# Performance work log

Hardware: AMD Instinct MI355X
Metric: run time of the kernel (lower is better)

The kernel has to match this reference:

```python
import jax, jax.numpy as jnp
import numpy as np

HIDDEN = 1024
ATTN = 1024
B, S = 4, 2048


def setup_inputs() -> dict:
    key = jax.random.key(0)
    ks = jax.random.split(key, 6)
    bound = 1.0 / np.sqrt(HIDDEN)
    return {
        "query": jax.random.normal(ks[0], (B, S, HIDDEN), jnp.float32),
        "value": jax.random.normal(ks[1], (B, S, HIDDEN), jnp.float32),
        "Wq": jax.random.uniform(ks[2], (HIDDEN, ATTN), jnp.float32, -bound, bound),
        "bq": jax.random.uniform(ks[3], (ATTN,), jnp.float32, -bound, bound),
        "Wv": jax.random.uniform(ks[4], (HIDDEN, ATTN), jnp.float32, -bound, bound),
        "bv": jax.random.uniform(ks[5], (ATTN,), jnp.float32, -bound, bound),
    }


def reference(query, value, Wq, bq, Wv, bv):
    # Linear projections (torch Linear: x @ W^T + b; here W stored as [in, out])
    q = jnp.einsum("bsh,hd->bsd", query, Wq) + bq  # [B,S,ATTN]
    v = jnp.einsum("bsh,hd->bsd", value, Wv) + bv  # [B,S,ATTN]
    # Unscaled dot-product attention
    scores = jnp.einsum("bqd,bkd->bqk", q, v)       # [B,S,S]
    attn = jax.nn.softmax(scores, axis=-1)
    context = jnp.einsum("bqk,bkd->bqd", attn, v)   # [B,S,ATTN]
    return context
```

## Files before the change

### kernel.cpp

```cpp
#include <hip/hip_runtime.h>
#include <hip/hip_bf16.h>


typedef unsigned short u16;
typedef __attribute__((ext_vector_type(8))) short bf16x8;
typedef __attribute__((ext_vector_type(4))) float f32x4;

typedef __attribute__((address_space(1))) void gvoid_t;
typedef __attribute__((address_space(3))) void svoid_t;

__device__ __forceinline__ void gll16(const void* g, void* l) {
    __builtin_amdgcn_global_load_lds((gvoid_t*)g, (svoid_t*)l, 16, 0, 0);
}

__device__ __forceinline__ u16 bf16rn(float x) {
    unsigned u = __float_as_uint(x);
    unsigned r = (u + 0x7FFFu + ((u >> 16) & 1u)) >> 16;
    return (u16)r;
}
__device__ __forceinline__ float bf2f(u16 h) {
    return __uint_as_float(((unsigned)h) << 16);
}

__device__ __forceinline__ const char* sel3(const char* p0, const char* p1,
                                            const char* p2, int i) {
    return i == 0 ? p0 : (i == 1 ? p1 : p2);
}

#define NSK 48

#define STAGE_A(T, mh) {                                                      \
    const char* _p = sel3(A0z, A1z, A2z, (T) >> 4) + (long)((T) & 15) * 128;  \
    char* _d = smem + (((T) & 1) << 16) + ((mh) << 14) + (w << 10);           \
    gll16(_p + offA##mh##0, _d);                                              \
    gll16(_p + offA##mh##1, _d + 8192); }

#define STAGE_B(T, nh) {                                                      \
    const char* _p = sel3(B0z, B1z, B2z, (T) >> 4) + (long)((T) & 15) * 128;  \
    char* _d = smem + (((T) & 1) << 16) + 32768 + ((nh) << 14) + (w << 10);   \
    gll16(_p + offB##nh##0, _d);                                              \
    gll16(_p + offB##nh##1, _d + 8192); }

#define VM4 { asm volatile("s_waitcnt vmcnt(4)" ::: "memory");                \
              __builtin_amdgcn_sched_barrier(0); }
#define VM0 { asm volatile("s_waitcnt vmcnt(0)" ::: "memory");                \
              __builtin_amdgcn_sched_barrier(0); }

#define PHASE(mh, nh, RDA, RDB, BFR, STAGE, ENDW)                             \
  {                                                                           \
    if (RDA) {                                                                \
      _Pragma("unroll") for (int mi = 0; mi < 4; ++mi)                        \
        _Pragma("unroll") for (int ks = 0; ks < 2; ++ks)                      \
          afr[mi][ks] = *(const bf16x8*)(smem + bufb + ((mh) << 14) +         \
              aRdB + mi * 2048 + csw[ks]);                                    \
    }                                                                         \
    if (RDB) {                                                                \
      _Pragma("unroll") for (int ni = 0; ni < 2; ++ni)                        \
        _Pragma("unroll") for (int ks = 0; ks < 2; ++ks)                      \
          BFR[ni][ks] = *(const bf16x8*)(smem + bufb + ((nh) << 14) +         \
              bRdB + ni * 2048 + csw[ks]);                                    \
    }                                                                         \
    STAGE;                                                                    \
    __builtin_amdgcn_s_barrier();                                             \
    asm volatile("s_waitcnt lgkmcnt(0)" ::: "memory");                        \
    __builtin_amdgcn_sched_barrier(0);                                        \
    __builtin_amdgcn_s_setprio(1);                                            \
    _Pragma("unroll") for (int mi = 0; mi < 4; ++mi)                          \
      _Pragma("unroll") for (int ni = 0; ni < 2; ++ni)                        \
        _Pragma("unroll") for (int ks = 0; ks < 2; ++ks)                      \
          acc[(mh) * 4 + mi][(nh) * 2 + ni] =                                 \
              __builtin_amdgcn_mfma_f32_16x16x32_bf16(                        \
                  afr[mi][ks], BFR[ni][ks],                                   \
                  acc[(mh) * 4 + mi][(nh) * 2 + ni], 0, 0, 0);                \
    __builtin_amdgcn_s_setprio(0);                                            \
    ENDW;                                                                     \
    __builtin_amdgcn_s_barrier();                                             \
  }

template<bool OUTF32, int SCHEME>
__global__ __launch_bounds__(512, 2)
void gemm8(const char* a0, const char* a1, const char* a2, long zA,
           const char* b0, const char* b1, const char* b2, long zB,
           float* __restrict__ Of, u16* __restrict__ Ohi, u16* __restrict__ Olo,
           long zC, const float* __restrict__ bias0,
           const float* __restrict__ bias1, int N)
{
    extern __shared__ char smem[];
    const int t = threadIdx.x, lane = t & 63, w = t >> 6;
    const int wm = w >> 2, wn = w & 3;

    const int bid = blockIdx.x;
    const int xcd = bid & 7, bi = bid >> 3;
    int m0, n0, z;
    if (SCHEME == 0) {
        z = xcd >> 1;
        m0 = (((xcd & 1) << 2) | (bi >> 3)) << 8;
        n0 = (bi & 7) << 8;
    } else {
        m0 = ((xcd << 2) | (bi >> 3)) << 8;
        n0 = (bi & 3) << 8;
        z = (bi >> 2) & 1;
    }

    const char* A0z = a0 + (long)z * zA;
    const char* A1z = a1 + (long)z * zA;
    const char* A2z = a2 + (long)z * zA;
    const char* B0z = b0 + (long)z * zB;
    const char* B1z = b1 + (long)z * zB;
    const char* B2z = b2 + (long)z * zB;

    const int lr0 = t >> 3;
    const long cg = (long)((((t & 7) ^ ((t >> 3) & 7)) << 4));
    const long offA00 = (long)(m0 + lr0) * 2048 + cg;
    const long offA01 = offA00 + 128L * 2048;
    const long offA10 = (long)(m0 + 64 + lr0) * 2048 + cg;
    const long offA11 = offA10 + 128L * 2048;
    const long offB00 = (long)(n0 + ((lr0 >> 5) << 6) + (lr0 & 31)) * 2048 + cg;
    const long offB01 = offB00 + 128L * 2048;
    const long offB10 = offB00 + 32L * 2048;
    const long offB11 = offB10 + 128L * 2048;

    const int swl = (lane & 7) << 4;
    const int csw[2] = { (((lane >> 4) << 4)) ^ swl,
                         (((lane >> 4) << 4) + 64) ^ swl };
    const int aRdB = (wm * 64 + (lane & 15)) * 128;
    const int bRdB = 32768 + (wn * 32 + (lane & 15)) * 128;

    f32x4 acc[8][4];
#pragma unroll
    for (int i = 0; i < 8; ++i)
#pragma unroll
        for (int j = 0; j < 4; ++j) acc[i][j] = (f32x4)0.f;
    bf16x8 afr[4][2];
    bf16x8 b0r[2][2], b1r[2][2];

    STAGE_A(0, 0); STAGE_B(0, 0); STAGE_A(0, 1); STAGE_B(0, 1);
    STAGE_A(1, 0); STAGE_B(1, 0);
    asm volatile("s_waitcnt vmcnt(4)" ::: "memory");
    __builtin_amdgcn_sched_barrier(0);
    __builtin_amdgcn_s_barrier();

    for (int s = 0; s < NSK - 2; ++s) {
        const int bufb = (s & 1) << 16;
        PHASE(0, 0, 1, 1, b0r, STAGE_A(s + 1, 1), );
        PHASE(0, 1, 0, 1, b1r, STAGE_B(s + 1, 1), );
        PHASE(1, 0, 1, 0, b0r, STAGE_A(s + 2, 0), );
        PHASE(1, 1, 0, 0, b1r, STAGE_B(s + 2, 0), VM4);
    }
    {
        const int bufb = ((NSK - 2) & 1) << 16;
        PHASE(0, 0, 1, 1, b0r, STAGE_A(NSK - 1, 1), );
        PHASE(0, 1, 0, 1, b1r, STAGE_B(NSK - 1, 1), );
        PHASE(1, 0, 1, 0, b0r, , );
        PHASE(1, 1, 0, 0, b1r, , VM0);
    }
    {
        const int bufb = ((NSK - 1) & 1) << 16;
        PHASE(0, 0, 1, 1, b0r, , );
        PHASE(0, 1, 0, 1, b1r, , );
        PHASE(1, 0, 1, 0, b0r, , );
        PHASE(1, 1, 0, 0, b1r, , );
    }

    const int r0 = m0 + wm * 128 + ((lane >> 4) << 2);
    const int c0 = n0 + wn * 64 + (lane & 15);
    if (OUTF32) {
        float* Co = Of + (long)z * zC;
#pragma unroll
        for (int mi = 0; mi < 8; ++mi)
#pragma unroll
            for (int nj = 0; nj < 4; ++nj)
#pragma unroll
                for (int r = 0; r < 4; ++r)
                    Co[(long)(r0 + mi * 16 + r) * N + c0 + nj * 16] =
                        acc[mi][nj][r];
    } else {
        const float* bs = z ? bias1 : bias0;
        float bc[4];
#pragma unroll
        for (int nj = 0; nj < 4; ++nj) bc[nj] = bs[c0 + nj * 16];
        u16* Oh = Ohi + (long)z * zC;
        u16* Ol = Olo + (long)z * zC;
#pragma unroll
        for (int mi = 0; mi < 8; ++mi)
#pragma unroll
            for (int nj = 0; nj < 4; ++nj)
#pragma unroll
                for (int r = 0; r < 4; ++r) {
                    float x = acc[mi][nj][r] + bc[nj];
                    long o = (long)(r0 + mi * 16 + r) * N + c0 + nj * 16;
                    u16 h = bf16rn(x);
                    Oh[o] = h;
                    Ol[o] = bf16rn(x - bf2f(h));
                }
    }
}

#define PVNSK 64

#define PV_STAGE_A(T, mh) {                                                   \
    const char* _p = Ap + (long)((T) & 31) * 128;                             \
    char* _d = smem + (((T) & 1) * 49152) + ((mh) << 14) + (w << 10);         \
    gll16(_p + offA##mh##0, _d);                                              \
    gll16(_p + offA##mh##1, _d + 8192); }

#define PV_STAGE_B(T, nh) {                                                   \
    const char* _p = (((T) >> 5) ? Bl : Bh) + (long)((T) & 31) * 128;         \
    char* _d = smem + (((T) & 1) * 49152) + 32768 + ((nh) << 13) + (w << 10); \
    gll16(_p + offB##nh, _d); }

#define PVM3 { asm volatile("s_waitcnt vmcnt(3)" ::: "memory");               \
               __builtin_amdgcn_sched_barrier(0); }

#define PVPHASE(mh, nh, RDA, RDB, BFR, STAGE, ENDW)                           \
  {                                                                           \
    if (RDA) {                                                                \
      _Pragma("unroll") for (int mi = 0; mi < 4; ++mi)                        \
        _Pragma("unroll") for (int ks = 0; ks < 2; ++ks)                      \
          afr[mi][ks] = *(const bf16x8*)(smem + bufb + ((mh) << 14) +         \
              aRdB + mi * 2048 + csw[ks]);                                    \
    }                                                                         \
    if (RDB) {                                                                \
      _Pragma("unroll") for (int ks = 0; ks < 2; ++ks)                        \
        BFR[ks] = *(const bf16x8*)(smem + bufb + 32768 + ((nh) << 13) +       \
            bRdB + csw[ks]);                                                  \
    }                                                                         \
    STAGE;                                                                    \
    __builtin_amdgcn_s_barrier();                                             \
    asm volatile("s_waitcnt lgkmcnt(0)" ::: "memory");                        \
    __builtin_amdgcn_sched_barrier(0);                                        \
    __builtin_amdgcn_s_setprio(1);                                            \
    _Pragma("unroll") for (int mi = 0; mi < 4; ++mi)                          \
      _Pragma("unroll") for (int ks = 0; ks < 2; ++ks)                        \
        acc[(mh) * 4 + mi][nh] =                                              \
            __builtin_amdgcn_mfma_f32_16x16x32_bf16(                          \
                afr[mi][ks], BFR[ks], acc[(mh) * 4 + mi][nh], 0, 0, 0);       \
    __builtin_amdgcn_s_setprio(0);                                            \
    ENDW;                                                                     \
    __builtin_amdgcn_s_barrier();                                             \
  }

__global__ __launch_bounds__(512, 2)
void gemm8pv(const char* pA, const char* vTh, const char* vTl,
             float* __restrict__ Of)
{
    extern __shared__ char smem[];
    const int t = threadIdx.x, lane = t & 63, w = t >> 6;
    const int wm = w >> 2, wn = w & 3;

    const int bid = blockIdx.x;
    const int xcd = bid & 7, bi = bid >> 3;
    const int z  = xcd >> 1;
    const int m0 = ((((xcd & 1) << 2) | (bi >> 3)) << 8);
    const int n0 = (bi & 7) << 7;

    const char* Ap = pA  + (long)z * 8388608;
    const char* Bh = vTh + (long)z * 4194304;
    const char* Bl = vTl + (long)z * 4194304;

    const int lr0 = t >> 3;
    const long cg = (long)((((t & 7) ^ ((t >> 3) & 7)) << 4));
    const long offA00 = (long)(m0 + lr0) * 4096 + cg;
    const long offA01 = offA00 + 64L * 4096;
    const long offA10 = (long)(m0 + 128 + lr0) * 4096 + cg;
    const long offA11 = offA10 + 64L * 4096;
    const long offB0  = (long)(n0 + lr0) * 4096 + cg;
    const long offB1  = (long)(n0 + 64 + lr0) * 4096 + cg;

    const int swl = (lane & 7) << 4;
    const int csw[2] = { (((lane >> 4) << 4)) ^ swl,
                         (((lane >> 4) << 4) + 64) ^ swl };
    const int aRdB = (wm * 64 + (lane & 15)) * 128;
    const int bRdB = (wn * 16 + (lane & 15)) * 128;

    f32x4 acc[8][2];
#pragma unroll
    for (int i = 0; i < 8; ++i) { acc[i][0] = (f32x4)0.f; acc[i][1] = (f32x4)0.f; }
    bf16x8 afr[4][2];
    bf16x8 bA[2], bB[2];

    PV_STAGE_A(0, 0); PV_STAGE_B(0, 0); PV_STAGE_A(0, 1); PV_STAGE_B(0, 1);
    PV_STAGE_A(1, 0); PV_STAGE_B(1, 0);
    asm volatile("s_waitcnt vmcnt(3)" ::: "memory");
    __builtin_amdgcn_sched_barrier(0);
    __builtin_amdgcn_s_barrier();

    for (int s = 0; s < PVNSK - 2; ++s) {
        const int bufb = (s & 1) * 49152;
        PVPHASE(0, 0, 1, 1, bA, PV_STAGE_A(s + 1, 1), );
        PVPHASE(0, 1, 0, 1, bB, PV_STAGE_B(s + 1, 1), );
        PVPHASE(1, 0, 1, 0, bA, PV_STAGE_A(s + 2, 0), );
        PVPHASE(1, 1, 0, 0, bB, PV_STAGE_B(s + 2, 0), PVM3);
    }
    {
        const int bufb = ((PVNSK - 2) & 1) * 49152;
        PVPHASE(0, 0, 1, 1, bA, PV_STAGE_A(PVNSK - 1, 1), );
        PVPHASE(0, 1, 0, 1, bB, PV_STAGE_B(PVNSK - 1, 1), );
        PVPHASE(1, 0, 1, 0, bA, , );
        PVPHASE(1, 1, 0, 0, bB, , VM0);
    }
    {
        const int bufb = ((PVNSK - 1) & 1) * 49152;
        PVPHASE(0, 0, 1, 1, bA, , );
        PVPHASE(0, 1, 0, 1, bB, , );
        PVPHASE(1, 0, 1, 0, bA, , );
        PVPHASE(1, 1, 0, 0, bB, , );
    }

    float* Co = Of + (long)z * 2097152;
    const int r0 = m0 + wm * 64 + ((lane >> 4) << 2);
    const int c0 = n0 + wn * 16 + (lane & 15);
#pragma unroll
    for (int mh = 0; mh < 2; ++mh)
#pragma unroll
        for (int mi = 0; mi < 4; ++mi)
#pragma unroll
            for (int nh = 0; nh < 2; ++nh)
#pragma unroll
                for (int r = 0; r < 4; ++r)
                    Co[(long)(r0 + mh * 128 + mi * 16 + r) * 1024 +
                       c0 + nh * 64] = acc[mh * 4 + mi][nh][r];
}

__global__ __launch_bounds__(256)
void split2_f32(const float* __restrict__ q, const float* __restrict__ v,
                u16* __restrict__ qh, u16* __restrict__ ql,
                u16* __restrict__ vh, u16* __restrict__ vl)
{
    const int sel = blockIdx.y;
    const float* in = sel ? v : q;
    u16* hi = sel ? vh : qh;
    u16* lo = sel ? vl : ql;
    long i = ((long)blockIdx.x * 256 + threadIdx.x) * 4;
    float4 x = *(const float4*)(in + i);
    ushort4 h, l;
    h.x = bf16rn(x.x); l.x = bf16rn(x.x - bf2f(h.x));
    h.y = bf16rn(x.y); l.y = bf16rn(x.y - bf2f(h.y));
    h.z = bf16rn(x.z); l.z = bf16rn(x.z - bf2f(h.z));
    h.w = bf16rn(x.w); l.w = bf16rn(x.w - bf2f(h.w));
    *(ushort4*)(hi + i) = h;
    *(ushort4*)(lo + i) = l;
}

__global__ __launch_bounds__(256)
void tsplit2_w(const float* __restrict__ Wq, const float* __restrict__ Wv,
               u16* __restrict__ qhi, u16* __restrict__ qlo,
               u16* __restrict__ vhi, u16* __restrict__ vlo)
{
    __shared__ float tile[32][33];
    const int sel = blockIdx.z;
    const float* W = sel ? Wv : Wq;
    u16* hi = sel ? vhi : qhi;
    u16* lo = sel ? vlo : qlo;
    const int n0v = blockIdx.x * 32, k0 = blockIdx.y * 32;
    const int r = threadIdx.x >> 5, c = threadIdx.x & 31;
#pragma unroll
    for (int it = 0; it < 4; ++it)
        tile[r + it * 8][c] = W[(long)(k0 + r + it * 8) * 1024 + n0v + c];
    __syncthreads();
#pragma unroll
    for (int it = 0; it < 4; ++it) {
        const int rr = r + it * 8;
        float x = tile[c][rr];
        u16 h = bf16rn(x);
        long o = (long)(n0v + rr) * 1024 + k0 + c;
        hi[o] = h;
        lo[o] = bf16rn(x - bf2f(h));
    }
}

__global__ __launch_bounds__(256)
void tr2_bf16(const u16* __restrict__ v_hi, const u16* __restrict__ v_lo,
              u16* __restrict__ vT_hi, u16* __restrict__ vT_lo)
{
    __shared__ u16 tile[64][68];
    const int pl = blockIdx.z & 1, b = blockIdx.z >> 1;
    const u16* src = (pl ? v_lo : v_hi) + (long)b * 2097152;
    u16* dst = (pl ? vT_lo : vT_hi) + (long)b * 2097152;
    const int s0 = blockIdx.x * 64, d0 = blockIdx.y * 64;
    const int t = threadIdx.x;
    const int rr = t >> 4, c4 = (t & 15) * 4;
#pragma unroll
    for (int it = 0; it < 4; ++it) {
        const int s = it * 16 + rr;
        *(short4*)&tile[s][c4] =
            *(const short4*)(src + (long)(s0 + s) * 1024 + d0 + c4);
    }
    __syncthreads();
#pragma unroll
    for (int it = 0; it < 4; ++it) {
        const int d = it * 16 + rr;
        short4 o;
        o.x = tile[c4 + 0][d]; o.y = tile[c4 + 1][d];
        o.z = tile[c4 + 2][d]; o.w = tile[c4 + 3][d];
        *(short4*)(dst + (long)(d0 + d) * 2048 + s0 + c4) = o;
    }
}

__global__ __launch_bounds__(256)
void softmax_p(const float* __restrict__ S, u16* __restrict__ P)
{
    const float* p = S + (long)blockIdx.x * 2048;
    u16* o = P + (long)blockIdx.x * 2048;
    const int t = threadIdx.x;

    float4 x0 = *(const float4*)&p[t * 4];
    float4 x1 = *(const float4*)&p[1024 + t * 4];

    float mx = fmaxf(fmaxf(fmaxf(x0.x, x0.y), fmaxf(x0.z, x0.w)),
                     fmaxf(fmaxf(x1.x, x1.y), fmaxf(x1.z, x1.w)));
#pragma unroll
    for (int off = 32; off; off >>= 1) mx = fmaxf(mx, __shfl_xor(mx, off));

    __shared__ float red[8];
    if ((t & 63) == 0) red[t >> 6] = mx;
    __syncthreads();
    mx = fmaxf(fmaxf(red[0], red[1]), fmaxf(red[2], red[3]));

    x0.x = __expf(x0.x - mx); x0.y = __expf(x0.y - mx);
    x0.z = __expf(x0.z - mx); x0.w = __expf(x0.w - mx);
    x1.x = __expf(x1.x - mx); x1.y = __expf(x1.y - mx);
    x1.z = __expf(x1.z - mx); x1.w = __expf(x1.w - mx);

    float sm2 = (x0.x + x0.y + x0.z + x0.w) + (x1.x + x1.y + x1.z + x1.w);
#pragma unroll
    for (int off = 32; off; off >>= 1) sm2 += __shfl_xor(sm2, off);
    if ((t & 63) == 0) red[4 + (t >> 6)] = sm2;
    __syncthreads();
    sm2 = (red[4] + red[5]) + (red[6] + red[7]);

    const float inv = 1.0f / sm2;
    ushort4 y;
    y.x = bf16rn(x0.x * inv); y.y = bf16rn(x0.y * inv);
    y.z = bf16rn(x0.z * inv); y.w = bf16rn(x0.w * inv);
    *(ushort4*)(o + t * 4) = y;
    y.x = bf16rn(x1.x * inv); y.y = bf16rn(x1.y * inv);
    y.z = bf16rn(x1.z * inv); y.w = bf16rn(x1.w * inv);
    *(ushort4*)(o + 1024 + t * 4) = y;
}

extern "C" void kernel_launch(void* const* d_in, const int* in_sizes, int n_in,
                              void* d_out, int out_size, void* d_ws, size_t ws_size,
                              hipStream_t stream)
{
    const float* query = (const float*)d_in[0];
    const float* value = (const float*)d_in[1];
    const float* Wq    = (const float*)d_in[2];
    const float* bq    = (const float*)d_in[3];
    const float* Wv    = (const float*)d_in[4];
    const float* bv    = (const float*)d_in[5];
    float* out = (float*)d_out;

    char* W = (char*)d_ws;
    u16* qx_hi = (u16*)(W);
    u16* qx_lo = qx_hi + 8388608;
    u16* vx_hi = qx_lo + 8388608;
    u16* vx_lo = vx_hi + 8388608;
    float* sc  = (float*)W;
    u16* q_hi  = (u16*)(W + 67108864);
    u16* q_lo  = q_hi + 8388608;
    u16* p     = (u16*)(W + 67108864);
    u16* v_hi  = (u16*)(W + 100663296);
    u16* v_lo  = v_hi + 8388608;
    u16* vT_hi = (u16*)(W + 134217728);
    u16* vT_lo = vT_hi + 8388608;
    u16* WqT_hi = (u16*)(W + 167772160);
    u16* WqT_lo = WqT_hi + 1048576;
    u16* WvT_hi = WqT_lo + 1048576;
    u16* WvT_lo = WvT_hi + 1048576;

    hipFuncSetAttribute((const void*)&gemm8<false, 1>,
                        hipFuncAttributeMaxDynamicSharedMemorySize, 131072);
    hipFuncSetAttribute((const void*)&gemm8<true, 0>,
                        hipFuncAttributeMaxDynamicSharedMemorySize, 131072);
    hipFuncSetAttribute((const void*)&gemm8pv,
                        hipFuncAttributeMaxDynamicSharedMemorySize, 98304);

    split2_f32<<<dim3(8192, 2), 256, 0, stream>>>(query, value,
                                                  qx_hi, qx_lo, vx_hi, vx_lo);
    tsplit2_w<<<dim3(32, 32, 2), 256, 0, stream>>>(Wq, Wv,
                                                   WqT_hi, WqT_lo, WvT_hi, WvT_lo);

    gemm8<false, 1><<<256, 512, 131072, stream>>>(
        (const char*)qx_hi, (const char*)qx_hi, (const char*)qx_lo, 33554432L,
        (const char*)WqT_hi, (const char*)WqT_lo, (const char*)WqT_hi, 4194304L,
        nullptr, q_hi, q_lo, 16777216L, bq, bv, 1024);

    tr2_bf16<<<dim3(32, 16, 8), 256, 0, stream>>>(v_hi, v_lo, vT_hi, vT_lo);

    gemm8<true, 0><<<256, 512, 131072, stream>>>(
        (const char*)q_hi, (const char*)q_hi, (const char*)q_lo, 4194304L,
        (const char*)v_hi, (const char*)v_lo, (const char*)v_hi, 4194304L,
        sc, nullptr, nullptr, 4194304L, nullptr, nullptr, 2048);

    softmax_p<<<8192, 256, 0, stream>>>(sc, p);

    gemm8pv<<<256, 512, 98304, stream>>>(
        (const char*)p, (const char*)vT_hi, (const char*)vT_lo, out);
}
```

Measured before the change: 393.5 us.

## Cut per-phase barriers in GEMM main loops to two per k-step

Replaces the four-phase structure, which had two workgroup barriers and an explicit LDS wait per phase, with straight-line reads, staging and MFMA quads. Each k-step now has only two barriers: one midway, before the second-half prefetch overwrites the half-buffer already consumed, and one at the end after the vmcnt wait. The LDS read waits are left to the compiler. This lowers barrier stalls and lets LDS reads overlap MFMAs, but it depends on the remaining barriers being enough to prevent write-after-read races on the shared buffers.

```diff
diff --git a/kernel.cpp b/kernel.cpp
--- a/kernel.cpp
+++ b/kernel.cpp
@@ -46,24 +46,19 @@
 #define VM0 { asm volatile("s_waitcnt vmcnt(0)" ::: "memory");                \
               __builtin_amdgcn_sched_barrier(0); }
 
-#define PHASE(mh, nh, RDA, RDB, BFR, STAGE, ENDW)                             \
-  {                                                                           \
-    if (RDA) {                                                                \
-      _Pragma("unroll") for (int mi = 0; mi < 4; ++mi)                        \
-        _Pragma("unroll") for (int ks = 0; ks < 2; ++ks)                      \
-          afr[mi][ks] = *(const bf16x8*)(smem + bufb + ((mh) << 14) +         \
-              aRdB + mi * 2048 + csw[ks]);                                    \
-    }                                                                         \
-    if (RDB) {                                                                \
-      _Pragma("unroll") for (int ni = 0; ni < 2; ++ni)                        \
-        _Pragma("unroll") for (int ks = 0; ks < 2; ++ks)                      \
-          BFR[ni][ks] = *(const bf16x8*)(smem + bufb + ((nh) << 14) +         \
-              bRdB + ni * 2048 + csw[ks]);                                    \
-    }                                                                         \
-    STAGE;                                                                    \
-    __builtin_amdgcn_s_barrier();                                             \
-    asm volatile("s_waitcnt lgkmcnt(0)" ::: "memory");                        \
-    __builtin_amdgcn_sched_barrier(0);                                        \
+#define RD_A(mh)                                                              \
+    _Pragma("unroll") for (int mi = 0; mi < 4; ++mi)                          \
+      _Pragma("unroll") for (int ks = 0; ks < 2; ++ks)                        \
+        afr[mi][ks] = *(const bf16x8*)(smem + bufb + ((mh) << 14) +           \
+            aRdB + mi * 2048 + csw[ks]);
+
+#define RD_B(BFR, nh)                                                         \
+    _Pragma("unroll") for (int ni = 0; ni < 2; ++ni)                          \
+      _Pragma("unroll") for (int ks = 0; ks < 2; ++ks)                        \
+        BFR[ni][ks] = *(const bf16x8*)(smem + bufb + ((nh) << 14) +           \
+            bRdB + ni * 2048 + csw[ks]);
+
+#define MFMA_Q(mh, nh, BFR) {                                                 \
     __builtin_amdgcn_s_setprio(1);                                            \
     _Pragma("unroll") for (int mi = 0; mi < 4; ++mi)                          \
       _Pragma("unroll") for (int ni = 0; ni < 2; ++ni)                        \
@@ -72,10 +67,7 @@
               __builtin_amdgcn_mfma_f32_16x16x32_bf16(                        \
                   afr[mi][ks], BFR[ni][ks],                                   \
                   acc[(mh) * 4 + mi][(nh) * 2 + ni], 0, 0, 0);                \
-    __builtin_amdgcn_s_setprio(0);                                            \
-    ENDW;                                                                     \
-    __builtin_amdgcn_s_barrier();                                             \
-  }
+    __builtin_amdgcn_s_setprio(0); }
 
 template<bool OUTF32, int SCHEME>
 __global__ __launch_bounds__(512, 2)
@@ -142,24 +134,44 @@
 
     for (int s = 0; s < NSK - 2; ++s) {
         const int bufb = (s & 1) << 16;
-        PHASE(0, 0, 1, 1, b0r, STAGE_A(s + 1, 1), );
-        PHASE(0, 1, 0, 1, b1r, STAGE_B(s + 1, 1), );
-        PHASE(1, 0, 1, 0, b0r, STAGE_A(s + 2, 0), );
-        PHASE(1, 1, 0, 0, b1r, STAGE_B(s + 2, 0), VM4);
+        RD_A(0); RD_B(b0r, 0);
+        STAGE_A(s + 1, 1);
+        MFMA_Q(0, 0, b0r);
+        RD_B(b1r, 1);
+        STAGE_B(s + 1, 1);
+        MFMA_Q(0, 1, b1r);
+        __builtin_amdgcn_s_barrier();
+        RD_A(1);
+        STAGE_A(s + 2, 0);
+        MFMA_Q(1, 0, b0r);
+        STAGE_B(s + 2, 0);
+        MFMA_Q(1, 1, b1r);
+        VM4;
+        __builtin_amdgcn_s_barrier();
     }
     {
         const int bufb = ((NSK - 2) & 1) << 16;
-        PHASE(0, 0, 1, 1, b0r, STAGE_A(NSK - 1, 1), );
-        PHASE(0, 1, 0, 1, b1r, STAGE_B(NSK - 1, 1), );
-        PHASE(1, 0, 1, 0, b0r, , );
-        PHASE(1, 1, 0, 0, b1r, , VM0);
+        RD_A(0); RD_B(b0r, 0);
+        STAGE_A(NSK - 1, 1);
+        MFMA_Q(0, 0, b0r);
+        RD_B(b1r, 1);
+        STAGE_B(NSK - 1, 1);
+        MFMA_Q(0, 1, b1r);
+        RD_A(1);
+        MFMA_Q(1, 0, b0r);
+        MFMA_Q(1, 1, b1r);
+        VM0;
+        __builtin_amdgcn_s_barrier();
     }
     {
         const int bufb = ((NSK - 1) & 1) << 16;
-        PHASE(0, 0, 1, 1, b0r, , );
-        PHASE(0, 1, 0, 1, b1r, , );
-        PHASE(1, 0, 1, 0, b0r, , );
-        PHASE(1, 1, 0, 0, b1r, , );
+        RD_A(0); RD_B(b0r, 0);
+        MFMA_Q(0, 0, b0r);
+        RD_B(b1r, 1);
+        MFMA_Q(0, 1, b1r);
+        RD_A(1);
+        MFMA_Q(1, 0, b0r);
+        MFMA_Q(1, 1, b1r);
     }
 
     const int r0 = m0 + wm * 128 + ((lane >> 4) << 2);
@@ -212,33 +224,25 @@
 #define PVM3 { asm volatile("s_waitcnt vmcnt(3)" ::: "memory");               \
                __builtin_amdgcn_sched_barrier(0); }
 
-#define PVPHASE(mh, nh, RDA, RDB, BFR, STAGE, ENDW)                           \
-  {                                                                           \
-    if (RDA) {                                                                \
-      _Pragma("unroll") for (int mi = 0; mi < 4; ++mi)                        \
-        _Pragma("unroll") for (int ks = 0; ks < 2; ++ks)                      \
-          afr[mi][ks] = *(const bf16x8*)(smem + bufb + ((mh) << 14) +         \
-              aRdB + mi * 2048 + csw[ks]);                                    \
-    }                                                                         \
-    if (RDB) {                                                                \
+#define PV_RD_A(mh)                                                           \
+    _Pragma("unroll") for (int mi = 0; mi < 4; ++mi)                          \
       _Pragma("unroll") for (int ks = 0; ks < 2; ++ks)                        \
-        BFR[ks] = *(const bf16x8*)(smem + bufb + 32768 + ((nh) << 13) +       \
-            bRdB + csw[ks]);                                                  \
-    }                                                                         \
-    STAGE;                                                                    \
-    __builtin_amdgcn_s_barrier();                                             \
-    asm volatile("s_waitcnt lgkmcnt(0)" ::: "memory");                        \
-    __builtin_amdgcn_sched_barrier(0);                                        \
+        afr[mi][ks] = *(const bf16x8*)(smem + bufb + ((mh) << 14) +           \
+            aRdB + mi * 2048 + csw[ks]);
+
+#define PV_RD_B(BFR, nh)                                                      \
+    _Pragma("unroll") for (int ks = 0; ks < 2; ++ks)                          \
+      BFR[ks] = *(const bf16x8*)(smem + bufb + 32768 + ((nh) << 13) +         \
+          bRdB + csw[ks]);
+
+#define PV_MFMA_Q(mh, nh, BFR) {                                              \
     __builtin_amdgcn_s_setprio(1);                                            \
     _Pragma("unroll") for (int mi = 0; mi < 4; ++mi)                          \
       _Pragma("unroll") for (int ks = 0; ks < 2; ++ks)                        \
         acc[(mh) * 4 + mi][nh] =                                              \
             __builtin_amdgcn_mfma_f32_16x16x32_bf16(                          \
                 afr[mi][ks], BFR[ks], acc[(mh) * 4 + mi][nh], 0, 0, 0);       \
-    __builtin_amdgcn_s_setprio(0);                                            \
-    ENDW;                                                                     \
-    __builtin_amdgcn_s_barrier();                                             \
-  }
+    __builtin_amdgcn_s_setprio(0); }
 
 __global__ __launch_bounds__(512, 2)
 void gemm8pv(const char* pA, const char* vTh, const char* vTl,
@@ -287,24 +291,44 @@
 
     for (int s = 0; s < PVNSK - 2; ++s) {
         const int bufb = (s & 1) * 49152;
-        PVPHASE(0, 0, 1, 1, bA, PV_STAGE_A(s + 1, 1), );
-        PVPHASE(0, 1, 0, 1, bB, PV_STAGE_B(s + 1, 1), );
-        PVPHASE(1, 0, 1, 0, bA, PV_STAGE_A(s + 2, 0), );
-        PVPHASE(1, 1, 0, 0, bB, PV_STAGE_B(s + 2, 0), PVM3);
+        PV_RD_A(0); PV_RD_B(bA, 0);
+        PV_STAGE_A(s + 1, 1);
+        PV_MFMA_Q(0, 0, bA);
+        PV_RD_B(bB, 1);
+        PV_STAGE_B(s + 1, 1);
+        PV_MFMA_Q(0, 1, bB);
+        __builtin_amdgcn_s_barrier();
+        PV_RD_A(1);
+        PV_STAGE_A(s + 2, 0);
+        PV_MFMA_Q(1, 0, bA);
+        PV_STAGE_B(s + 2, 0);
+        PV_MFMA_Q(1, 1, bB);
+        PVM3;
+        __builtin_amdgcn_s_barrier();
     }
     {
         const int bufb = ((PVNSK - 2) & 1) * 49152;
-        PVPHASE(0, 0, 1, 1, bA, PV_STAGE_A(PVNSK - 1, 1), );
-        PVPHASE(0, 1, 0, 1, bB, PV_STAGE_B(PVNSK - 1, 1), );
-        PVPHASE(1, 0, 1, 0, bA, , );
-        PVPHASE(1, 1, 0, 0, bB, , VM0);
+        PV_RD_A(0); PV_RD_B(bA, 0);
+        PV_STAGE_A(PVNSK - 1, 1);
+        PV_MFMA_Q(0, 0, bA);
+        PV_RD_B(bB, 1);
+        PV_STAGE_B(PVNSK - 1, 1);
+        PV_MFMA_Q(0, 1, bB);
+        PV_RD_A(1);
+        PV_MFMA_Q(1, 0, bA);
+        PV_MFMA_Q(1, 1, bB);
+        VM0;
+        __builtin_amdgcn_s_barrier();
     }
     {
         const int bufb = ((PVNSK - 1) & 1) * 49152;
-        PVPHASE(0, 0, 1, 1, bA, , );
-        PVPHASE(0, 1, 0, 1, bB, , );
-        PVPHASE(1, 0, 1, 0, bA, , );
-        PVPHASE(1, 1, 0, 0, bB, , );
+        PV_RD_A(0); PV_RD_B(bA, 0);
+        PV_MFMA_Q(0, 0, bA);
+        PV_RD_B(bB, 1);
+        PV_MFMA_Q(0, 1, bB);
+        PV_RD_A(1);
+        PV_MFMA_Q(1, 0, bA);
+        PV_MFMA_Q(1, 1, bB);
     }
 
     float* Co = Of + (long)z * 2097152;
```

Result: faster. 379.6 us (-3.5%).
